# Kernel optimization log

Measured on AMD Instinct MI355X. Metric: run time of the kernel, lower is better.

## Reference

```python
import jax, jax.numpy as jnp
import numpy as np
import math

N = 200000      # active voxels
M = 80000       # rule pairs per kernel offset
K = 27          # 3^3 kernel offsets
INC, OUTC = 64, 128   # supernet max channels
RIN, ROUT = 48, 96    # runtime (sampled) channels


def setup_inputs() -> dict:
    key = jax.random.key(0)
    k1, k2, k3, k4 = jax.random.split(key, 4)
    features = jax.random.normal(k1, (N, RIN), dtype=jnp.float32)
    std = 1.0 / math.sqrt(INC * K)  # matches init_weight (non-transposed)
    kernel = jax.random.uniform(k2, (K, INC, OUTC), dtype=jnp.float32,
                                minval=-std, maxval=std)
    in_map = jax.random.randint(k3, (K, M), 0, N, dtype=jnp.int32)
    out_map = jax.random.randint(k4, (K, M), 0, N, dtype=jnp.int32)
    return {"features": features, "kernel": kernel,
            "in_map": in_map, "out_map": out_map,
            "rin": RIN, "rout": ROUT}


def reference(features, kernel, in_map, out_map, rin, rout):
    # Dynamic channel slicing: kernel[:, arange(rin), :][..., arange(rout)]
    w = kernel[:, :rin, :rout]                      # [K, rin, rout]
    # Gather-GEMM-scatter rulebook sparse conv (torchsparse spf.conv3d):
    gathered = features[in_map]                     # [K, M, rin]
    contrib = jnp.einsum('kmi,kio->kmo', gathered, w)  # [K, M, rout]
    out = jnp.zeros((features.shape[0], rout), dtype=features.dtype)
    out = out.at[out_map.reshape(-1)].add(contrib.reshape(-1, rout))
    return out
```

## Files before the change

### kernel.cpp

```cpp
#include <hip/hip_runtime.h>
#include <hip/hip_bf16.h>

#define KK   27
#define MM   80000
#define NN   200000
#define INC  64
#define OUTC 128
#define RIN  48
#define ROUT 96

#define SLICE   40
#define NSLICE  (NN / SLICE)
#define NKEY    (KK * NSLICE)

#define HEPB    4096
#define HBLK    ((MM + HEPB - 1) / HEPB)
#define NC      (NKEY * HBLK)
#define ETOT    (KK * MM)

#define SCHUNK  1024
#define NCB     ((NC + SCHUNK - 1) / SCHUNK)
#define MIDW    11

#define CHUNK   768

typedef __attribute__((ext_vector_type(8))) short bf16x8;
typedef __attribute__((ext_vector_type(4))) float f32x4;

__device__ __forceinline__ float bf2f(short s) {
    return __uint_as_float(((unsigned)(unsigned short)s) << 16);
}

#define FB_BLOCKS_PER_K 200
#define FB_ENTRIES_PER_BLOCK ((MM + FB_BLOCKS_PER_K - 1) / FB_BLOCKS_PER_K)

__global__ __launch_bounds__(192)
void sparse_conv_scatter(const float* __restrict__ feat,
                         const float* __restrict__ w,
                         const int* __restrict__ imap,
                         const int* __restrict__ omap,
                         float* __restrict__ out)
{
    __shared__ float wlds[RIN * ROUT];
    const int k = blockIdx.y;
    const float* wk = w + (size_t)k * INC * OUTC;
    for (int idx = threadIdx.x; idx < RIN * ROUT; idx += 192) {
        int i = idx / ROUT;
        int o = idx - i * ROUT;
        wlds[idx] = wk[i * OUTC + o];
    }
    __syncthreads();

    const int sub = threadIdx.x / 96;
    const int oc  = threadIdx.x % 96;
    const int m0 = blockIdx.x * FB_ENTRIES_PER_BLOCK;
    const int m1 = min(m0 + FB_ENTRIES_PER_BLOCK, MM);
    const int* imk = imap + (size_t)k * MM;
    const int* omk = omap + (size_t)k * MM;

    for (int m = m0 + sub; m < m1; m += 2) {
        const int fin  = imk[m];
        const int fout = omk[m];
        const float4* f4 = (const float4*)(feat + (size_t)fin * RIN);
        float acc = 0.f;
        #pragma unroll
        for (int i4 = 0; i4 < RIN / 4; ++i4) {
            float4 v = f4[i4];
            acc += v.x * wlds[(i4 * 4 + 0) * ROUT + oc];
            acc += v.y * wlds[(i4 * 4 + 1) * ROUT + oc];
            acc += v.z * wlds[(i4 * 4 + 2) * ROUT + oc];
            acc += v.w * wlds[(i4 * 4 + 3) * ROUT + oc];
        }
        atomicAdd(&out[(size_t)fout * ROUT + oc], acc);
    }
}

__global__ __launch_bounds__(256)
void feat_to_bf16(const float* __restrict__ f, __hip_bfloat16* __restrict__ fb)
{
    const size_t i = (size_t)blockIdx.x * 256 + threadIdx.x;
    if (i >= (size_t)NN * RIN / 8) return;
    const float4* p = (const float4*)(f + i * 8);
    float4 a = p[0], b = p[1];
    union { __hip_bfloat16 h[8]; uint4 v; } o;
    o.h[0] = __float2bfloat16(a.x);
    o.h[1] = __float2bfloat16(a.y);
    o.h[2] = __float2bfloat16(a.z);
    o.h[3] = __float2bfloat16(a.w);
    o.h[4] = __float2bfloat16(b.x);
    o.h[5] = __float2bfloat16(b.y);
    o.h[6] = __float2bfloat16(b.z);
    o.h[7] = __float2bfloat16(b.w);
    ((uint4*)fb)[i] = o.v;
}

__global__ __launch_bounds__(64)
void build_wpack(const float* __restrict__ w, __hip_bfloat16* __restrict__ wp)
{
    const int b = blockIdx.x;
    const int k = b / 12;
    const int f = b % 12;
    const int oct = f / 2, ktile = f % 2;
    const int lane = threadIdx.x;
    const int oc    = oct * 16 + (lane & 15);
    const int kbase = ktile * 32 + (lane >> 4) * 8;
    union { __hip_bfloat16 h[8]; uint4 v; } o;
    #pragma unroll
    for (int j = 0; j < 8; ++j) {
        int ki = kbase + j;
        float val = (ki < RIN) ? w[(size_t)k * INC * OUTC + (size_t)ki * OUTC + oc] : 0.f;
        o.h[j] = __float2bfloat16(val);
    }
    ((uint4*)wp)[(size_t)b * 64 + lane] = o.v;
}

__global__ __launch_bounds__(256)
void hist_pass(const int* __restrict__ omap, int* __restrict__ C)
{
    __shared__ int h[NSLICE];
    const int k = blockIdx.y;
    const int blk = blockIdx.x;
    for (int i = threadIdx.x; i < NSLICE; i += 256) h[i] = 0;
    __syncthreads();

    #pragma unroll
    for (int it = 0; it < HEPB / 256; ++it) {
        const int m = blk * HEPB + it * 256 + threadIdx.x;
        if (m < MM) atomicAdd(&h[omap[(size_t)k * MM + m] / SLICE], 1);
    }
    __syncthreads();
    for (int i = threadIdx.x; i < NSLICE; i += 256)
        C[((size_t)k * NSLICE + i) * HBLK + blk] = h[i];
}

__global__ __launch_bounds__(256)
void scan_part2(const int* __restrict__ C, int* __restrict__ S)
{
    __shared__ int sh[256];
    const int t = threadIdx.x;
    const int base = blockIdx.x * SCHUNK + t * 4;
    int s = 0;
    #pragma unroll
    for (int j = 0; j < 4; ++j)
        if (base + j < NC) s += C[base + j];
    sh[t] = s;
    __syncthreads();
    for (int off = 128; off > 0; off >>= 1) {
        if (t < off) sh[t] += sh[t + off];
        __syncthreads();
    }
    if (t == 0) S[blockIdx.x] = sh[0];
}

__global__ __launch_bounds__(256)
void scan_mid(int* __restrict__ S)
{
    __shared__ int sh[256];
    const int t = threadIdx.x;
    int v[MIDW];
    int tot = 0;
    #pragma unroll
    for (int j = 0; j < MIDW; ++j) {
        const int idx = t * MIDW + j;
        v[j] = (idx < NCB) ? S[idx] : 0;
        tot += v[j];
    }
    sh[t] = tot;
    __syncthreads();
    for (int off = 1; off < 256; off <<= 1) {
        int x = (t >= off) ? sh[t - off] : 0;
        __syncthreads();
        sh[t] += x;
        __syncthreads();
    }
    int run = sh[t] - tot;
    #pragma unroll
    for (int j = 0; j < MIDW; ++j) {
        const int idx = t * MIDW + j;
        if (idx < NCB) { const int tv = v[j]; S[idx] = run; run += tv; }
    }
}

__global__ __launch_bounds__(256)
void scan_final2(int* __restrict__ C, const int* __restrict__ S)
{
    __shared__ int sh[256];
    const int t = threadIdx.x;
    const int base = blockIdx.x * SCHUNK + t * 4;
    int v[4];
    int s = 0;
    #pragma unroll
    for (int j = 0; j < 4; ++j) {
        v[j] = (base + j < NC) ? C[base + j] : 0;
        s += v[j];
    }
    sh[t] = s;
    __syncthreads();
    for (int off = 1; off < 256; off <<= 1) {
        int x = (t >= off) ? sh[t - off] : 0;
        __syncthreads();
        sh[t] += x;
        __syncthreads();
    }
    int run = sh[t] - s + S[blockIdx.x];
    #pragma unroll
    for (int j = 0; j < 4; ++j) {
        if (base + j < NC) { C[base + j] = run; run += v[j]; }
    }
}

__global__ __launch_bounds__(256)
void write_elist(const int* __restrict__ omap,
                 const int* __restrict__ imap,
                 const int* __restrict__ Cs,
                 unsigned* __restrict__ elist)
{
    __shared__ int run[NSLICE];
    const int k = blockIdx.y;
    const int blk = blockIdx.x;
    for (int i = threadIdx.x; i < NSLICE; i += 256) run[i] = 0;
    __syncthreads();

    #pragma unroll
    for (int it = 0; it < HEPB / 256; ++it) {
        const int m = blk * HEPB + it * 256 + threadIdx.x;
        if (m < MM) {
            const size_t e = (size_t)k * MM + m;
            const int r = omap[e];
            const int s = r / SLICE;
            const int lr = r - s * SLICE;
            const int rank = atomicAdd(&run[s], 1);
            const int base = Cs[((size_t)k * NSLICE + s) * HBLK + blk];
            elist[base + rank] = (unsigned)imap[e] | ((unsigned)lr << 18);
        }
    }
}

__global__ __launch_bounds__(256)
void stage1_mfma(const __hip_bfloat16* __restrict__ fb,
                 const __hip_bfloat16* __restrict__ wp,
                 const unsigned* __restrict__ elist,
                 const int* __restrict__ Cs,
                 int t, int spr, int capseg,
                 __hip_bfloat16* __restrict__ contrib)
{
    const int k = blockIdx.y;
    const int wid  = threadIdx.x >> 6;
    const int lane = threadIdx.x & 63;
    const int lo = lane & 15, hi = lane >> 4;

    const size_t key0 = (size_t)k * NSLICE + (size_t)t * spr;
    const size_t key1 = key0 + spr;
    const int seg0 = Cs[key0 * HBLK];
    const int seg1 = (key1 < NKEY) ? Cs[key1 * HBLK] : ETOT;
    const int n = seg1 - seg0;
    const int ntiles = (n + 15) >> 4;

    bf16x8 B[12];
    #pragma unroll
    for (int f = 0; f < 12; ++f)
        B[f] = *reinterpret_cast<const bf16x8*>(
            (const char*)wp + (((size_t)k * 12 + f) * 64 + lane) * 16);

    const int wstride = gridDim.x * 4;
    const int t0 = blockIdx.x * 4 + wid;
    if (t0 >= ntiles) return;

    auto LOADA = [&](int tile, bf16x8& a0, bf16x8& a1) {
        const int ea = seg0 + tile * 16 + lo;
        const unsigned tg = (tile < ntiles && ea < seg1) ? elist[ea] : 0u;
        const int row = (int)(tg & 0x3FFFFu);
        a0 = *reinterpret_cast<const bf16x8*>((const char*)fb + (size_t)row * 96 + hi * 16);
        a1 = *reinterpret_cast<const bf16x8*>((const char*)fb + (size_t)row * 96 + 64 + hi * 16);
    };

    bf16x8 A0, A1, P0, P1, Q0, Q1;
    LOADA(t0, A0, A1);
    LOADA(t0 + wstride, P0, P1);

    for (int tile = t0; tile < ntiles; tile += wstride) {
        LOADA(tile + 2 * wstride, Q0, Q1);

        const int e4 = tile * 16 + hi * 4;
        const size_t sbase = (size_t)k * capseg + e4;
        const bool v0 = (e4 + 0) < n, v1 = (e4 + 1) < n,
                   v2 = (e4 + 2) < n, v3 = (e4 + 3) < n;

        #pragma unroll
        for (int oct = 0; oct < 6; ++oct) {
            f32x4 a = {0.f, 0.f, 0.f, 0.f};
            a = __builtin_amdgcn_mfma_f32_16x16x32_bf16(A0, B[oct * 2 + 0], a, 0, 0, 0);
            a = __builtin_amdgcn_mfma_f32_16x16x32_bf16(A1, B[oct * 2 + 1], a, 0, 0, 0);
            const int oc = oct * 16 + lo;
            if (v0) contrib[(sbase + 0) * ROUT + oc] = __float2bfloat16(a[0]);
            if (v1) contrib[(sbase + 1) * ROUT + oc] = __float2bfloat16(a[1]);
            if (v2) contrib[(sbase + 2) * ROUT + oc] = __float2bfloat16(a[2]);
            if (v3) contrib[(sbase + 3) * ROUT + oc] = __float2bfloat16(a[3]);
        }

        A0 = P0; A1 = P1;
        P0 = Q0; P1 = Q1;
    }
}

__global__ __launch_bounds__(512)
void stage2_sorted(const __hip_bfloat16* __restrict__ contrib,
                   const unsigned* __restrict__ elist,
                   const int* __restrict__ Cs,
                   int t, int spr, int capseg,
                   float* __restrict__ out)
{
    __shared__ int kb0[KK], klb[KK];
    __shared__ int koff[KK + 1];
    __shared__ int rowcnt[SLICE];
    __shared__ int rowoff[SLICE + 1];
    __shared__ int srcSorted[CHUNK];

    const int sl  = t * spr + blockIdx.x;
    const int tid = threadIdx.x;

    if (tid < KK) {
        const int k = tid;
        const size_t key = (size_t)k * NSLICE + sl;
        const int b0 = Cs[key * HBLK];
        const int b1 = (key + 1 < NKEY) ? Cs[(key + 1) * HBLK] : ETOT;
        const int segb = Cs[((size_t)k * NSLICE + (size_t)t * spr) * HBLK];
        kb0[k]  = b0;
        klb[k]  = k * capseg + (b0 - segb);
        koff[k] = b1 - b0;
    }
    __syncthreads();
    if (tid == 0) {
        int run = 0;
        for (int k = 0; k < KK; ++k) { const int c = koff[k]; koff[k] = run; run += c; }
        koff[KK] = run;
    }
    __syncthreads();
    const int nE = koff[KK];

    const int lr = tid / 12;
    const int g  = tid - lr * 12;
    const bool owner = (tid < SLICE * 12);

    f32x4 accA = {0.f, 0.f, 0.f, 0.f};
    f32x4 accB = {0.f, 0.f, 0.f, 0.f};

    for (int c0 = 0; c0 < nE; c0 += CHUNK) {
        const int ce = min(nE - c0, CHUNK);

        if (tid < SLICE) rowcnt[tid] = 0;
        __syncthreads();

        int myLr[2], myRank[2], mySrc[2];
        int nmine = 0;
        for (int i = tid; i < ce; i += 512) {
            const int ge = c0 + i;
            int lo = 0, hi = KK;
            while (hi - lo > 1) {
                const int mid = (lo + hi) >> 1;
                if (ge >= koff[mid]) lo = mid; else hi = mid;
            }
            const int j = ge - koff[lo];
            const int l = (int)(elist[kb0[lo] + j] >> 18);
            myLr[nmine]   = l;
            mySrc[nmine]  = klb[lo] + j;
            myRank[nmine] = atomicAdd(&rowcnt[l], 1);
            ++nmine;
        }
        __syncthreads();

        if (tid == 0) {
            int run = 0;
            for (int r = 0; r < SLICE; ++r) { rowoff[r] = run; run += rowcnt[r]; }
            rowoff[SLICE] = run;
        }
        __syncthreads();

        for (int q = 0; q < nmine; ++q)
            srcSorted[rowoff[myLr[q]] + myRank[q]] = mySrc[q];
        __syncthreads();

        if (owner) {
            const int j0 = rowoff[lr], j1 = rowoff[lr + 1];
            for (int j = j0; j < j1; ++j) {
                const bf16x8 v = *reinterpret_cast<const bf16x8*>(
                    contrib + (size_t)srcSorted[j] * ROUT + g * 8);
                accA[0] += bf2f(v[0]); accA[1] += bf2f(v[1]);
                accA[2] += bf2f(v[2]); accA[3] += bf2f(v[3]);
                accB[0] += bf2f(v[4]); accB[1] += bf2f(v[5]);
                accB[2] += bf2f(v[6]); accB[3] += bf2f(v[7]);
            }
        }
        __syncthreads();
    }

    if (owner) {
        float4* o = (float4*)(out + ((size_t)sl * SLICE + lr) * ROUT + g * 8);
        float4 x0 = {accA[0], accA[1], accA[2], accA[3]};
        float4 x1 = {accB[0], accB[1], accB[2], accB[3]};
        o[0] = x0; o[1] = x1;
    }
}

extern "C" void kernel_launch(void* const* d_in, const int* in_sizes, int n_in,
                              void* d_out, int out_size, void* d_ws, size_t ws_size,
                              hipStream_t stream)
{
    const float* features = (const float*)d_in[0];
    const float* kernel_w = (const float*)d_in[1];
    const int*   in_map   = (const int*)d_in[2];
    const int*   out_map  = (const int*)d_in[3];
    float*       out      = (float*)d_out;

    const size_t off_C       = 0;
    const size_t off_S       = off_C + (((size_t)NC * 4 + 255) & ~255ul);
    const size_t off_fb      = off_S + (((size_t)NCB * 4 + 255) & ~255ul);
    const size_t off_wp      = off_fb + (size_t)NN * RIN * 2;
    const size_t off_elist   = off_wp + (size_t)KK * 12 * 64 * 16;
    const size_t off_contrib = off_elist + (((size_t)ETOT + 64) * 4);

    int nt = 0, capseg = 0;
    {
        const size_t need4 = off_contrib + (size_t)KK * 21504 * ROUT * 2;
        if (ws_size >= need4) { nt = 4; capseg = 21504; }
    }

    if (nt == 0) {
        hipMemsetAsync(d_out, 0, (size_t)out_size * sizeof(float), stream);
        dim3 grid(FB_BLOCKS_PER_K, KK);
        sparse_conv_scatter<<<grid, 192, 0, stream>>>(features, kernel_w, in_map, out_map, out);
        return;
    }

    const int spr = NSLICE / nt;
    const int s1x = 240 / nt;

    char* ws = (char*)d_ws;
    int*      C     = (int*)(ws + off_C);
    int*      S     = (int*)(ws + off_S);
    __hip_bfloat16* fb = (__hip_bfloat16*)(ws + off_fb);
    __hip_bfloat16* wp = (__hip_bfloat16*)(ws + off_wp);
    unsigned* elist = (unsigned*)(ws + off_elist);
    __hip_bfloat16* contrib = (__hip_bfloat16*)(ws + off_contrib);

    feat_to_bf16<<<(NN * RIN / 8 + 255) / 256, 256, 0, stream>>>(features, fb);
    build_wpack<<<KK * 12, 64, 0, stream>>>(kernel_w, wp);

    {
        dim3 gh(HBLK, KK);
        hist_pass<<<gh, 256, 0, stream>>>(out_map, C);
    }
    scan_part2<<<NCB, 256, 0, stream>>>(C, S);
    scan_mid<<<1, 256, 0, stream>>>(S);
    scan_final2<<<NCB, 256, 0, stream>>>(C, S);
    {
        dim3 gw(HBLK, KK);
        write_elist<<<gw, 256, 0, stream>>>(out_map, in_map, C, elist);
    }

    for (int t = 0; t < nt; ++t) {
        dim3 g1(s1x, KK);
        stage1_mfma<<<g1, 256, 0, stream>>>(fb, wp, elist, C, t, spr, capseg, contrib);
        stage2_sorted<<<spr, 512, 0, stream>>>(contrib, elist, C, t, spr, capseg, out);
    }
}
```

Before: 411.0 us.

## Restructure counting-sort prefix scan into per-slice block scan plus small key scan

The histogram layout becomes block-major per kernel offset, so histogram writes are contiguous. A new blk_scan kernel scans across the 20 histogram blocks for each slice, and the three-pass global scan then runs only over the per-key totals (about 135K entries) instead of all key×block counts (about 2.7M). write_elist caches per-slice base offsets in shared memory instead of doing a global lookup per element. This is meant to cut the scan traffic and the strided global reads in the rulebook-sorting phase, at the cost of one extra kernel launch and a serial 20-step loop per thread.

```diff
diff --git a/kernel.cpp b/kernel.cpp
--- a/kernel.cpp
+++ b/kernel.cpp
@@ -15,12 +15,10 @@
 
 #define HEPB    4096
 #define HBLK    ((MM + HEPB - 1) / HEPB)
-#define NC      (NKEY * HBLK)
 #define ETOT    (KK * MM)
 
 #define SCHUNK  1024
-#define NCB     ((NC + SCHUNK - 1) / SCHUNK)
-#define MIDW    11
+#define NCB2    ((NKEY + SCHUNK - 1) / SCHUNK)
 
 #define CHUNK   768
 
@@ -115,7 +113,7 @@
 }
 
 __global__ __launch_bounds__(256)
-void hist_pass(const int* __restrict__ omap, int* __restrict__ C)
+void hist_pass(const int* __restrict__ omap, int* __restrict__ L)
 {
     __shared__ int h[NSLICE];
     const int k = blockIdx.y;
@@ -129,12 +127,29 @@
         if (m < MM) atomicAdd(&h[omap[(size_t)k * MM + m] / SLICE], 1);
     }
     __syncthreads();
-    for (int i = threadIdx.x; i < NSLICE; i += 256)
-        C[((size_t)k * NSLICE + i) * HBLK + blk] = h[i];
-}
-
-__global__ __launch_bounds__(256)
-void scan_part2(const int* __restrict__ C, int* __restrict__ S)
+    int* row = L + ((size_t)k * HBLK + blk) * NSLICE;
+    for (int i = threadIdx.x; i < NSLICE; i += 256) row[i] = h[i];
+}
+
+__global__ __launch_bounds__(256)
+void blk_scan(int* __restrict__ L, int* __restrict__ T)
+{
+    const int k = blockIdx.y;
+    const int s = blockIdx.x * 256 + threadIdx.x;
+    if (s >= NSLICE) return;
+    int run = 0;
+    #pragma unroll
+    for (int blk = 0; blk < HBLK; ++blk) {
+        const size_t idx = ((size_t)k * HBLK + blk) * NSLICE + s;
+        const int v = L[idx];
+        L[idx] = run;
+        run += v;
+    }
+    T[(size_t)k * NSLICE + s] = run;
+}
+
+__global__ __launch_bounds__(256)
+void scan_partG(const int* __restrict__ T, int* __restrict__ S, int n)
 {
     __shared__ int sh[256];
     const int t = threadIdx.x;
@@ -142,7 +157,7 @@
     int s = 0;
     #pragma unroll
     for (int j = 0; j < 4; ++j)
-        if (base + j < NC) s += C[base + j];
+        if (base + j < n) s += T[base + j];
     sh[t] = s;
     __syncthreads();
     for (int off = 128; off > 0; off >>= 1) {
@@ -153,18 +168,15 @@
 }
 
 __global__ __launch_bounds__(256)
-void scan_mid(int* __restrict__ S)
+void scan_midG(int* __restrict__ S, int ncb)
 {
     __shared__ int sh[256];
     const int t = threadIdx.x;
-    int v[MIDW];
+    const int per = (ncb + 255) / 256;
+    const int lo = t * per;
+    const int hi = min(lo + per, ncb);
     int tot = 0;
-    #pragma unroll
-    for (int j = 0; j < MIDW; ++j) {
-        const int idx = t * MIDW + j;
-        v[j] = (idx < NCB) ? S[idx] : 0;
-        tot += v[j];
-    }
+    for (int i = lo; i < hi; ++i) tot += S[i];
     sh[t] = tot;
     __syncthreads();
     for (int off = 1; off < 256; off <<= 1) {
@@ -174,15 +186,11 @@
         __syncthreads();
     }
     int run = sh[t] - tot;
-    #pragma unroll
-    for (int j = 0; j < MIDW; ++j) {
-        const int idx = t * MIDW + j;
-        if (idx < NCB) { const int tv = v[j]; S[idx] = run; run += tv; }
-    }
-}
-
-__global__ __launch_bounds__(256)
-void scan_final2(int* __restrict__ C, const int* __restrict__ S)
+    for (int i = lo; i < hi; ++i) { const int v = S[i]; S[i] = run; run += v; }
+}
+
+__global__ __launch_bounds__(256)
+void scan_finalG(int* __restrict__ T, const int* __restrict__ S, int n, int total)
 {
     __shared__ int sh[256];
     const int t = threadIdx.x;
@@ -191,7 +199,7 @@
     int s = 0;
     #pragma unroll
     for (int j = 0; j < 4; ++j) {
-        v[j] = (base + j < NC) ? C[base + j] : 0;
+        v[j] = (base + j < n) ? T[base + j] : 0;
         s += v[j];
     }
     sh[t] = s;
@@ -205,20 +213,29 @@
     int run = sh[t] - s + S[blockIdx.x];
     #pragma unroll
     for (int j = 0; j < 4; ++j) {
-        if (base + j < NC) { C[base + j] = run; run += v[j]; }
-    }
+        if (base + j < n) { T[base + j] = run; run += v[j]; }
+    }
+    if (blockIdx.x == 0 && t == 0) T[n] = total;
 }
 
 __global__ __launch_bounds__(256)
 void write_elist(const int* __restrict__ omap,
                  const int* __restrict__ imap,
-                 const int* __restrict__ Cs,
+                 const int* __restrict__ B,
+                 const int* __restrict__ L,
                  unsigned* __restrict__ elist)
 {
+    __shared__ int basev[NSLICE];
     __shared__ int run[NSLICE];
     const int k = blockIdx.y;
     const int blk = blockIdx.x;
-    for (int i = threadIdx.x; i < NSLICE; i += 256) run[i] = 0;
+
+    const int* Bk = B + (size_t)k * NSLICE;
+    const int* Lk = L + ((size_t)k * HBLK + blk) * NSLICE;
+    for (int i = threadIdx.x; i < NSLICE; i += 256) {
+        basev[i] = Bk[i] + Lk[i];
+        run[i] = 0;
+    }
     __syncthreads();
 
     #pragma unroll
@@ -230,8 +247,7 @@
             const int s = r / SLICE;
             const int lr = r - s * SLICE;
             const int rank = atomicAdd(&run[s], 1);
-            const int base = Cs[((size_t)k * NSLICE + s) * HBLK + blk];
-            elist[base + rank] = (unsigned)imap[e] | ((unsigned)lr << 18);
+            elist[basev[s] + rank] = (unsigned)imap[e] | ((unsigned)lr << 18);
         }
     }
 }
@@ -240,7 +256,7 @@
 void stage1_mfma(const __hip_bfloat16* __restrict__ fb,
                  const __hip_bfloat16* __restrict__ wp,
                  const unsigned* __restrict__ elist,
-                 const int* __restrict__ Cs,
+                 const int* __restrict__ B,
                  int t, int spr, int capseg,
                  __hip_bfloat16* __restrict__ contrib)
 {
@@ -250,16 +266,15 @@
     const int lo = lane & 15, hi = lane >> 4;
 
     const size_t key0 = (size_t)k * NSLICE + (size_t)t * spr;
-    const size_t key1 = key0 + spr;
-    const int seg0 = Cs[key0 * HBLK];
-    const int seg1 = (key1 < NKEY) ? Cs[key1 * HBLK] : ETOT;
+    const int seg0 = B[key0];
+    const int seg1 = B[key0 + spr];
     const int n = seg1 - seg0;
     const int ntiles = (n + 15) >> 4;
 
-    bf16x8 B[12];
+    bf16x8 Bf[12];
     #pragma unroll
     for (int f = 0; f < 12; ++f)
-        B[f] = *reinterpret_cast<const bf16x8*>(
+        Bf[f] = *reinterpret_cast<const bf16x8*>(
             (const char*)wp + (((size_t)k * 12 + f) * 64 + lane) * 16);
 
     const int wstride = gridDim.x * 4;
@@ -289,8 +304,8 @@
         #pragma unroll
         for (int oct = 0; oct < 6; ++oct) {
             f32x4 a = {0.f, 0.f, 0.f, 0.f};
-            a = __builtin_amdgcn_mfma_f32_16x16x32_bf16(A0, B[oct * 2 + 0], a, 0, 0, 0);
-            a = __builtin_amdgcn_mfma_f32_16x16x32_bf16(A1, B[oct * 2 + 1], a, 0, 0, 0);
+            a = __builtin_amdgcn_mfma_f32_16x16x32_bf16(A0, Bf[oct * 2 + 0], a, 0, 0, 0);
+            a = __builtin_amdgcn_mfma_f32_16x16x32_bf16(A1, Bf[oct * 2 + 1], a, 0, 0, 0);
             const int oc = oct * 16 + lo;
             if (v0) contrib[(sbase + 0) * ROUT + oc] = __float2bfloat16(a[0]);
             if (v1) contrib[(sbase + 1) * ROUT + oc] = __float2bfloat16(a[1]);
@@ -306,7 +321,7 @@
 __global__ __launch_bounds__(512)
 void stage2_sorted(const __hip_bfloat16* __restrict__ contrib,
                    const unsigned* __restrict__ elist,
-                   const int* __restrict__ Cs,
+                   const int* __restrict__ B,
                    int t, int spr, int capseg,
                    float* __restrict__ out)
 {
@@ -322,9 +337,9 @@
     if (tid < KK) {
         const int k = tid;
         const size_t key = (size_t)k * NSLICE + sl;
-        const int b0 = Cs[key * HBLK];
-        const int b1 = (key + 1 < NKEY) ? Cs[(key + 1) * HBLK] : ETOT;
-        const int segb = Cs[((size_t)k * NSLICE + (size_t)t * spr) * HBLK];
+        const int b0 = B[key];
+        const int b1 = B[key + 1];
+        const int segb = B[(size_t)k * NSLICE + (size_t)t * spr];
         kb0[k]  = b0;
         klb[k]  = k * capseg + (b0 - segb);
         koff[k] = b1 - b0;
@@ -412,9 +427,10 @@
     const int*   out_map  = (const int*)d_in[3];
     float*       out      = (float*)d_out;
 
-    const size_t off_C       = 0;
-    const size_t off_S       = off_C + (((size_t)NC * 4 + 255) & ~255ul);
-    const size_t off_fb      = off_S + (((size_t)NCB * 4 + 255) & ~255ul);
+    const size_t off_L       = 0;
+    const size_t off_B       = off_L + (((size_t)KK * HBLK * NSLICE * 4 + 255) & ~255ul);
+    const size_t off_S       = off_B + (((size_t)(NKEY + 1) * 4 + 255) & ~255ul);
+    const size_t off_fb      = off_S + 1024;
     const size_t off_wp      = off_fb + (size_t)NN * RIN * 2;
     const size_t off_elist   = off_wp + (size_t)KK * 12 * 64 * 16;
     const size_t off_contrib = off_elist + (((size_t)ETOT + 64) * 4);
@@ -436,7 +452,8 @@
     const int s1x = 240 / nt;
 
     char* ws = (char*)d_ws;
-    int*      C     = (int*)(ws + off_C);
+    int*      L     = (int*)(ws + off_L);
+    int*      B     = (int*)(ws + off_B);
     int*      S     = (int*)(ws + off_S);
     __hip_bfloat16* fb = (__hip_bfloat16*)(ws + off_fb);
     __hip_bfloat16* wp = (__hip_bfloat16*)(ws + off_wp);
@@ -448,19 +465,23 @@
 
     {
         dim3 gh(HBLK, KK);
-        hist_pass<<<gh, 256, 0, stream>>>(out_map, C);
-    }
-    scan_part2<<<NCB, 256, 0, stream>>>(C, S);
-    scan_mid<<<1, 256, 0, stream>>>(S);
-    scan_final2<<<NCB, 256, 0, stream>>>(C, S);
+        hist_pass<<<gh, 256, 0, stream>>>(out_map, L);
+    }
+    {
+        dim3 gb((NSLICE + 255) / 256, KK);
+        blk_scan<<<gb, 256, 0, stream>>>(L, B);
+    }
+    scan_partG<<<NCB2, 256, 0, stream>>>(B, S, NKEY);
+    scan_midG<<<1, 256, 0, stream>>>(S, NCB2);
+    scan_finalG<<<NCB2, 256, 0, stream>>>(B, S, NKEY, ETOT);
     {
         dim3 gw(HBLK, KK);
-        write_elist<<<gw, 256, 0, stream>>>(out_map, in_map, C, elist);
+        write_elist<<<gw, 256, 0, stream>>>(out_map, in_map, B, L, elist);
     }
 
     for (int t = 0; t < nt; ++t) {
         dim3 g1(s1x, KK);
-        stage1_mfma<<<g1, 256, 0, stream>>>(fb, wp, elist, C, t, spr, capseg, contrib);
-        stage2_sorted<<<spr, 512, 0, stream>>>(contrib, elist, C, t, spr, capseg, out);
-    }
-}
+        stage1_mfma<<<g1, 256, 0, stream>>>(fb, wp, elist, B, t, spr, capseg, contrib);
+        stage2_sorted<<<spr, 512, 0, stream>>>(contrib, elist, B, t, spr, capseg, out);
+    }
+}
```

Result: faster. 356.2 us (-13.3%).
